# Kernel optimization log

Measured on AMD Instinct MI355X. Metric: run time of the kernel, lower is better.

The kernel has to match this reference:

```python
import jax, jax.numpy as jnp
import numpy as np

# --- constants (match init_kwargs / input_specs) ---
N_NODES = 32768   # total nodes
N_EDGES = 262144  # total edges (avg degree 8)
B = 512           # number of graphs
D = 64            # node feature / hidden dim (scalar irreps width)
DE = 16           # edge attribute dim
NEXP = 8          # num_experts
K = 2             # top-k


def setup_inputs() -> dict:
    key = jax.random.key(0)
    ks = jax.random.split(key, 20)
    x = jax.random.normal(ks[0], (N_NODES, D), dtype=jnp.float32)
    edge_src = jax.random.randint(ks[1], (N_EDGES,), 0, N_NODES, dtype=jnp.int32)
    edge_dst = jax.random.randint(ks[2], (N_EDGES,), 0, N_NODES, dtype=jnp.int32)
    edge_attr = jax.random.normal(ks[3], (N_EDGES, DE), dtype=jnp.float32)
    # sorted graph ids, every graph non-empty (64 nodes each)
    batch = jnp.repeat(jnp.arange(B, dtype=jnp.int32), N_NODES // B)
    s = 1.0 / np.sqrt(D)
    se = 1.0 / np.sqrt(DE)
    # embedding GNN params
    emb_We = jax.random.normal(ks[4], (DE, D), dtype=jnp.float32) * se
    emb_W1 = jax.random.normal(ks[5], (D, D), dtype=jnp.float32) * s
    emb_W2 = jax.random.normal(ks[6], (D, D), dtype=jnp.float32) * s
    emb_b = jnp.zeros((D,), dtype=jnp.float32)
    # gating network
    Wg = jax.random.normal(ks[7], (D, NEXP), dtype=jnp.float32) * s
    bg = jnp.zeros((NEXP,), dtype=jnp.float32)
    # stacked expert params [NEXP, ...]
    ex_We = jax.random.normal(ks[8], (NEXP, DE, D), dtype=jnp.float32) * se
    ex_W1 = jax.random.normal(ks[9], (NEXP, D, D), dtype=jnp.float32) * s
    ex_W2 = jax.random.normal(ks[10], (NEXP, D, D), dtype=jnp.float32) * s
    ex_b = jnp.zeros((NEXP, D), dtype=jnp.float32)
    ex_Wout = jax.random.normal(ks[11], (NEXP, D, 1), dtype=jnp.float32) * s
    ex_bout = jnp.zeros((NEXP, 1), dtype=jnp.float32)
    return {
        "x": x, "edge_attr": edge_attr,
        "emb_We": emb_We, "emb_W1": emb_W1, "emb_W2": emb_W2, "emb_b": emb_b,
        "Wg": Wg, "bg": bg,
        "ex_We": ex_We, "ex_W1": ex_W1, "ex_W2": ex_W2, "ex_b": ex_b,
        "ex_Wout": ex_Wout, "ex_bout": ex_bout,
        "edge_src": edge_src, "edge_dst": edge_dst, "batch": batch,
    }


def _gnn_embed(x, edge_attr, We, W1, W2, b, src, dst, batch):
    # edge-gated messages: gather x[src], modulate by projected edge attrs, scatter to dst
    msg = x[src] * (edge_attr @ We)                          # [E, D]
    agg = jax.ops.segment_sum(msg, dst, num_segments=N_NODES)  # [N, D]
    h = jax.nn.relu(x @ W1 + agg @ W2 + b)                   # [N, D]
    # mean pooling per graph
    gsum = jax.ops.segment_sum(h, batch, num_segments=B)      # [B, D]
    cnt = jax.ops.segment_sum(jnp.ones((N_NODES, 1), h.dtype), batch, num_segments=B)
    return gsum / jnp.maximum(cnt, 1.0)                      # [B, D]


def _expert(x, edge_attr, We, W1, W2, b, Wout, bout, src, dst, batch):
    emb = _gnn_embed(x, edge_attr, We, W1, W2, b, src, dst, batch)
    return emb @ Wout + bout                                  # [B, 1]


def reference(x, edge_attr, emb_We, emb_W1, emb_W2, emb_b, Wg, bg,
              ex_We, ex_W1, ex_W2, ex_b, ex_Wout, ex_bout,
              edge_src, edge_dst, batch):
    # 1) graph embeddings via embedding GNN
    graph_emb = _gnn_embed(x, edge_attr, emb_We, emb_W1, emb_W2, emb_b,
                           edge_src, edge_dst, batch)          # [B, D]
    # 2) gating: softmax over experts, top-k, renormalize
    routing_weights = jax.nn.softmax(graph_emb @ Wg + bg, axis=1)  # [B, NEXP]
    top_k_weights, top_k_indices = jax.lax.top_k(routing_weights, K)
    norm_top_k = jax.nn.softmax(top_k_weights, axis=1)             # [B, K]
    # 3) dispatch: run every expert on the full batch (vectorized equivalent of
    #    the per-expert masked sub-batch loop), then gather routed outputs
    expert_outs = jax.vmap(
        lambda We, W1, W2, b, Wo, bo: _expert(
            x, edge_attr, We, W1, W2, b, Wo, bo, edge_src, edge_dst, batch)
    )(ex_We, ex_W1, ex_W2, ex_b, ex_Wout, ex_bout)             # [NEXP, B, 1]
    per_graph = expert_outs[:, :, 0].T                         # [B, NEXP]
    gathered = jnp.take_along_axis(per_graph, top_k_indices, axis=1)  # [B, K]
    # 4) weighted combine
    final_output = jnp.sum(gathered * norm_top_k, axis=1, keepdims=True)  # [B, 1]
    return final_output, routing_weights
```

## Files before the change

### kernel.cpp

```cpp
#include <hip/hip_runtime.h>

#define N_NODES 32768
#define N_EDGES 262144
#define NB      512
#define D       64
#define DE      16
#define NEXP    8

typedef __attribute__((ext_vector_type(8))) short  short8v;
typedef __attribute__((ext_vector_type(4))) float  floatx4;

static __device__ __forceinline__ unsigned short f2bf(float f) {
  unsigned int u = __float_as_uint(f);
  u += 0x7FFFu + ((u >> 16) & 1u);
  return (unsigned short)(u >> 16);
}


__global__ void hist_kernel(const int* __restrict__ dst, int* __restrict__ counts) {
  int i = blockIdx.x * blockDim.x + threadIdx.x;
  if (i < N_EDGES) atomicAdd(&counts[dst[i]], 1);
}

__global__ void scan1_kernel(const int* __restrict__ counts, int* __restrict__ offsets,
                             int* __restrict__ bsums) {
  __shared__ int sm[256];
  int t = threadIdx.x, i = blockIdx.x * 256 + t;
  int v = counts[i];
  sm[t] = v;
  __syncthreads();
  for (int off = 1; off < 256; off <<= 1) {
    int u = (t >= off) ? sm[t - off] : 0;
    __syncthreads();
    sm[t] += u;
    __syncthreads();
  }
  offsets[i] = sm[t] - v;
  if (t == 255) bsums[blockIdx.x] = sm[255];
}

__global__ void scan2_kernel(int* __restrict__ bsums) {
  __shared__ int sm[128];
  int t = threadIdx.x;
  int v = bsums[t];
  sm[t] = v;
  __syncthreads();
  for (int off = 1; off < 128; off <<= 1) {
    int u = (t >= off) ? sm[t - off] : 0;
    __syncthreads();
    sm[t] += u;
    __syncthreads();
  }
  bsums[t] = sm[t] - v;
}

__global__ void scan3_kernel(int* __restrict__ offsets, const int* __restrict__ bsums,
                             int* __restrict__ cursor) {
  int i = blockIdx.x * 256 + threadIdx.x;
  int v = offsets[i] + bsums[blockIdx.x];
  offsets[i] = v;
  cursor[i]  = v;
  if (i == 0) offsets[N_NODES] = N_EDGES;
}

__global__ void scatter_kernel(const int* __restrict__ dst, const int* __restrict__ src,
                               const float4* __restrict__ ea4, int* __restrict__ cursor,
                               int* __restrict__ sorted_src, float4* __restrict__ sea4) {
  int i = blockIdx.x * blockDim.x + threadIdx.x;
  if (i < N_EDGES) {
    int p = atomicAdd(&cursor[dst[i]], 1);
    sorted_src[p] = src[i];
    float4 a = ea4[(size_t)i * 4 + 0];
    float4 b = ea4[(size_t)i * 4 + 1];
    float4 c = ea4[(size_t)i * 4 + 2];
    float4 d = ea4[(size_t)i * 4 + 3];
    sea4[(size_t)p * 4 + 0] = a;
    sea4[(size_t)p * 4 + 1] = b;
    sea4[(size_t)p * 4 + 2] = c;
    sea4[(size_t)p * 4 + 3] = d;
  }
}


__global__ void xconv_kernel(const float4* __restrict__ x4, ushort4* __restrict__ xb4) {
  int i = blockIdx.x * blockDim.x + threadIdx.x;
  float4 v = x4[i];
  ushort4 o;
  o.x = f2bf(v.x); o.y = f2bf(v.y); o.z = f2bf(v.z); o.w = f2bf(v.w);
  xb4[i] = o;
}

__global__ void wpack_kernel(const float* __restrict__ ex_W1, const float* __restrict__ ex_W2,
                             unsigned short* __restrict__ wpk) {
  int idx = blockIdx.x * 256 + threadIdx.x;
  int je  = idx >> 13;
  int rem = idx & 8191;
  int mat = rem >> 12;
  int cd  = rem & 4095;
  int col = cd >> 6, k = cd & 63;
  const float* W = mat ? ex_W2 : ex_W1;
  wpk[idx] = f2bf(W[je * 4096 + k * 64 + col]);
}


__global__ __launch_bounds__(256) void agg_kernel(
    const float* __restrict__ x, const int* __restrict__ sorted_src,
    const float4* __restrict__ sea4, const int* __restrict__ offsets,
    const float* __restrict__ emb_We, const float* __restrict__ ex_We,
    float* __restrict__ agg0, unsigned short* __restrict__ aggb) {
  int lane = threadIdx.x & 63;
  int n = blockIdx.x * 4 + (threadIdx.x >> 6);
  int st = offsets[n], en = offsets[n + 1];
  float t[DE];
#pragma unroll
  for (int k = 0; k < DE; ++k) t[k] = 0.f;
  for (int i = st; i < en; ++i) {
    int s = sorted_src[i];
    float xv = x[(size_t)s * D + lane];
    float4 e0 = sea4[(size_t)i * 4 + 0];
    float4 e1 = sea4[(size_t)i * 4 + 1];
    float4 e2 = sea4[(size_t)i * 4 + 2];
    float4 e3 = sea4[(size_t)i * 4 + 3];
    t[0]  += xv * e0.x; t[1]  += xv * e0.y; t[2]  += xv * e0.z; t[3]  += xv * e0.w;
    t[4]  += xv * e1.x; t[5]  += xv * e1.y; t[6]  += xv * e1.z; t[7]  += xv * e1.w;
    t[8]  += xv * e2.x; t[9]  += xv * e2.y; t[10] += xv * e2.z; t[11] += xv * e2.w;
    t[12] += xv * e3.x; t[13] += xv * e3.y; t[14] += xv * e3.z; t[15] += xv * e3.w;
  }
  {
    float a = 0.f;
#pragma unroll
    for (int k = 0; k < DE; ++k) a += t[k] * emb_We[k * D + lane];
    agg0[(size_t)n * D + lane] = a;
  }
  for (int je = 0; je < NEXP; ++je) {
    const float* We = ex_We + (size_t)je * DE * D;
    float a = 0.f;
#pragma unroll
    for (int k = 0; k < DE; ++k) a += t[k] * We[k * D + lane];
    aggb[((size_t)je * N_NODES + n) * D + lane] = f2bf(a);
  }
}


__global__ __launch_bounds__(256) void gnn0_kernel(
    const float* __restrict__ x, const float* __restrict__ agg0,
    const float* __restrict__ W1, const float* __restrict__ W2,
    const float* __restrict__ bvv, float* __restrict__ graph_emb) {
  __shared__ __align__(16) float w1s[D * D];
  __shared__ __align__(16) float w2s[D * D];
  __shared__ __align__(16) float xs[D * D];
  __shared__ __align__(16) float as2[D * D];
  int b = blockIdx.x;
  int t = threadIdx.x;
  const float4* w1src = (const float4*)W1;
  const float4* w2src = (const float4*)W2;
  const float4* xsrc  = (const float4*)(x    + (size_t)b * D * D);
  const float4* asrc  = (const float4*)(agg0 + (size_t)b * D * D);
#pragma unroll
  for (int r = 0; r < 4; ++r) {
    ((float4*)w1s)[t + r * 256] = w1src[t + r * 256];
    ((float4*)w2s)[t + r * 256] = w2src[t + r * 256];
    ((float4*)xs)[t + r * 256]  = xsrc[t + r * 256];
    ((float4*)as2)[t + r * 256] = asrc[t + r * 256];
  }
  int w = t >> 6, lane = t & 63;
  float bias = bvv[lane];
  __syncthreads();
  float pool = 0.f;
#pragma unroll
  for (int q = 0; q < 4; ++q) {
    int n0 = w * 16 + q * 4;
    float a0 = bias, a1 = bias, a2 = bias, a3 = bias;
#pragma unroll 4
    for (int c4 = 0; c4 < 16; ++c4) {
      float4 x0 = *(const float4*)&xs[(n0 + 0) * D + c4 * 4];
      float4 x1 = *(const float4*)&xs[(n0 + 1) * D + c4 * 4];
      float4 x2 = *(const float4*)&xs[(n0 + 2) * D + c4 * 4];
      float4 x3 = *(const float4*)&xs[(n0 + 3) * D + c4 * 4];
      float4 g0 = *(const float4*)&as2[(n0 + 0) * D + c4 * 4];
      float4 g1 = *(const float4*)&as2[(n0 + 1) * D + c4 * 4];
      float4 g2 = *(const float4*)&as2[(n0 + 2) * D + c4 * 4];
      float4 g3 = *(const float4*)&as2[(n0 + 3) * D + c4 * 4];
      float w10 = w1s[(c4 * 4 + 0) * D + lane];
      float w11 = w1s[(c4 * 4 + 1) * D + lane];
      float w12 = w1s[(c4 * 4 + 2) * D + lane];
      float w13 = w1s[(c4 * 4 + 3) * D + lane];
      float w20 = w2s[(c4 * 4 + 0) * D + lane];
      float w21 = w2s[(c4 * 4 + 1) * D + lane];
      float w22 = w2s[(c4 * 4 + 2) * D + lane];
      float w23 = w2s[(c4 * 4 + 3) * D + lane];
      a0 += x0.x * w10 + x0.y * w11 + x0.z * w12 + x0.w * w13
          + g0.x * w20 + g0.y * w21 + g0.z * w22 + g0.w * w23;
      a1 += x1.x * w10 + x1.y * w11 + x1.z * w12 + x1.w * w13
          + g1.x * w20 + g1.y * w21 + g1.z * w22 + g1.w * w23;
      a2 += x2.x * w10 + x2.y * w11 + x2.z * w12 + x2.w * w13
          + g2.x * w20 + g2.y * w21 + g2.z * w22 + g2.w * w23;
      a3 += x3.x * w10 + x3.y * w11 + x3.z * w12 + x3.w * w13
          + g3.x * w20 + g3.y * w21 + g3.z * w22 + g3.w * w23;
    }
    pool += fmaxf(a0, 0.f) + fmaxf(a1, 0.f) + fmaxf(a2, 0.f) + fmaxf(a3, 0.f);
  }
  __syncthreads();
  xs[w * D + lane] = pool;
  __syncthreads();
  if (w == 0) {
    float s = xs[lane] + xs[D + lane] + xs[2 * D + lane] + xs[3 * D + lane];
    graph_emb[b * D + lane] = s * (1.f / 64.f);
  }
}


__global__ __launch_bounds__(256) void gnn_mfma_kernel(
    const unsigned short* __restrict__ xb, const unsigned short* __restrict__ aggb,
    const unsigned short* __restrict__ wpk,
    const float* __restrict__ ex_b, const float* __restrict__ ex_Wout,
    const float* __restrict__ ex_bout, float* __restrict__ per_graph) {
  int g = blockIdx.x;
  int wv = threadIdx.x >> 6;
  int je = blockIdx.y * 4 + wv;
  int lane = threadIdx.x & 63;
  int r = lane & 15, q = lane >> 4;

  const short* Xb = (const short*)(xb   + (size_t)g * D * D);
  const short* Ab = (const short*)(aggb + ((size_t)je * N_NODES + (size_t)g * D) * D);
  const short* B1 = (const short*)(wpk + (size_t)je * 2 * 4096);
  const short* B2 = B1 + 4096;

  floatx4 acc[4][4];
#pragma unroll
  for (int i = 0; i < 4; ++i)
#pragma unroll
    for (int j = 0; j < 4; ++j) acc[i][j] = (floatx4){0.f, 0.f, 0.f, 0.f};

#pragma unroll
  for (int kk = 0; kk < 2; ++kk) {
    int ko = kk * 32 + q * 8;
    short8v af[4], bf[4];
#pragma unroll
    for (int rt = 0; rt < 4; ++rt) af[rt] = *(const short8v*)(Xb + (rt * 16 + r) * D + ko);
#pragma unroll
    for (int ct = 0; ct < 4; ++ct) bf[ct] = *(const short8v*)(B1 + (ct * 16 + r) * D + ko);
#pragma unroll
    for (int rt = 0; rt < 4; ++rt)
#pragma unroll
      for (int ct = 0; ct < 4; ++ct)
        acc[rt][ct] = __builtin_amdgcn_mfma_f32_16x16x32_bf16(af[rt], bf[ct], acc[rt][ct], 0, 0, 0);
  }
#pragma unroll
  for (int kk = 0; kk < 2; ++kk) {
    int ko = kk * 32 + q * 8;
    short8v af[4], bf[4];
#pragma unroll
    for (int rt = 0; rt < 4; ++rt) af[rt] = *(const short8v*)(Ab + (rt * 16 + r) * D + ko);
#pragma unroll
    for (int ct = 0; ct < 4; ++ct) bf[ct] = *(const short8v*)(B2 + (ct * 16 + r) * D + ko);
#pragma unroll
    for (int rt = 0; rt < 4; ++rt)
#pragma unroll
      for (int ct = 0; ct < 4; ++ct)
        acc[rt][ct] = __builtin_amdgcn_mfma_f32_16x16x32_bf16(af[rt], bf[ct], acc[rt][ct], 0, 0, 0);
  }

  float o = 0.f;
#pragma unroll
  for (int ct = 0; ct < 4; ++ct) {
    float bcol = ex_b[je * D + ct * 16 + r];
    float s = 0.f;
#pragma unroll
    for (int rt = 0; rt < 4; ++rt)
#pragma unroll
      for (int rg = 0; rg < 4; ++rg) s += fmaxf(acc[rt][ct][rg] + bcol, 0.f);
    s += __shfl_xor(s, 16);
    s += __shfl_xor(s, 32);
    o += s * ex_Wout[je * D + ct * 16 + r];
  }
#pragma unroll
  for (int off = 8; off >= 1; off >>= 1) o += __shfl_xor(o, off);
  if (lane == 0) per_graph[g * NEXP + je] = o * (1.f / 64.f) + ex_bout[je];
}


__global__ void gate_kernel(const float* __restrict__ graph_emb, const float* __restrict__ Wg,
                            const float* __restrict__ bg, const float* __restrict__ per_graph,
                            float* __restrict__ out) {
  __shared__ float es[D];
  __shared__ float lg[NEXP];
  int b = blockIdx.x, lane = threadIdx.x;
  es[lane] = graph_emb[b * D + lane];
  __syncthreads();
  if (lane < NEXP) {
    float v = bg[lane];
    for (int d = 0; d < D; ++d) v += es[d] * Wg[d * NEXP + lane];
    lg[lane] = v;
  }
  __syncthreads();
  float l[NEXP];
  float mx = -1e30f;
#pragma unroll
  for (int e = 0; e < NEXP; ++e) { l[e] = lg[e]; mx = fmaxf(mx, l[e]); }
  float p[NEXP];
  float sum = 0.f;
#pragma unroll
  for (int e = 0; e < NEXP; ++e) { p[e] = expf(l[e] - mx); sum += p[e]; }
  float inv = 1.f / sum;
#pragma unroll
  for (int e = 0; e < NEXP; ++e) p[e] *= inv;
  if (lane < NEXP) out[NB + b * NEXP + lane] = p[lane];
  if (lane == 0) {
    int i1 = -1; float v1 = -1e30f;
#pragma unroll
    for (int e = 0; e < NEXP; ++e) if (p[e] > v1) { v1 = p[e]; i1 = e; }
    int i2 = -1; float v2 = -1e30f;
#pragma unroll
    for (int e = 0; e < NEXP; ++e) if (e != i1 && p[e] > v2) { v2 = p[e]; i2 = e; }
    float rr = expf(v2 - v1);
    float n1 = 1.f / (1.f + rr);
    float n2 = rr / (1.f + rr);
    out[b] = n1 * per_graph[b * NEXP + i1] + n2 * per_graph[b * NEXP + i2];
  }
}


extern "C" void kernel_launch(void* const* d_in, const int* in_sizes, int n_in,
                              void* d_out, int out_size, void* d_ws, size_t ws_size,
                              hipStream_t stream) {
  const float* x         = (const float*)d_in[0];
  const float* edge_attr = (const float*)d_in[1];
  const float* emb_We    = (const float*)d_in[2];
  const float* emb_W1    = (const float*)d_in[3];
  const float* emb_W2    = (const float*)d_in[4];
  const float* emb_b     = (const float*)d_in[5];
  const float* Wg        = (const float*)d_in[6];
  const float* bg        = (const float*)d_in[7];
  const float* ex_We     = (const float*)d_in[8];
  const float* ex_W1     = (const float*)d_in[9];
  const float* ex_W2     = (const float*)d_in[10];
  const float* ex_b      = (const float*)d_in[11];
  const float* ex_Wout   = (const float*)d_in[12];
  const float* ex_bout   = (const float*)d_in[13];
  const int* edge_src    = (const int*)d_in[14];
  const int* edge_dst    = (const int*)d_in[15];

  char* p = (char*)d_ws;
  auto alloc = [&](size_t bytes) {
    char* q = p;
    p += (bytes + 255) & ~(size_t)255;
    return q;
  };
  int*   counts     = (int*)alloc((size_t)N_NODES * 4);
  int*   offsets    = (int*)alloc((size_t)(N_NODES + 1) * 4);
  int*   cursor     = (int*)alloc((size_t)N_NODES * 4);
  int*   bsums      = (int*)alloc(128 * 4);
  int*   sorted_src = (int*)alloc((size_t)N_EDGES * 4);
  float* sorted_ea  = (float*)alloc((size_t)N_EDGES * DE * 4);
  float* agg0       = (float*)alloc((size_t)N_NODES * D * 4);
  unsigned short* aggb = (unsigned short*)alloc((size_t)NEXP * N_NODES * D * 2);
  unsigned short* xb   = (unsigned short*)alloc((size_t)N_NODES * D * 2);
  unsigned short* wpk  = (unsigned short*)alloc((size_t)NEXP * 2 * D * D * 2);
  float* graph_emb  = (float*)alloc((size_t)NB * D * 4);
  float* per_graph  = (float*)alloc((size_t)NB * NEXP * 4);

  hipMemsetAsync(counts, 0, (size_t)N_NODES * 4, stream);
  hist_kernel<<<N_EDGES / 256, 256, 0, stream>>>(edge_dst, counts);
  scan1_kernel<<<N_NODES / 256, 256, 0, stream>>>(counts, offsets, bsums);
  scan2_kernel<<<1, 128, 0, stream>>>(bsums);
  scan3_kernel<<<N_NODES / 256, 256, 0, stream>>>(offsets, bsums, cursor);
  scatter_kernel<<<N_EDGES / 256, 256, 0, stream>>>(edge_dst, edge_src,
                                                    (const float4*)edge_attr, cursor,
                                                    sorted_src, (float4*)sorted_ea);
  xconv_kernel<<<(N_NODES * D / 4) / 256, 256, 0, stream>>>((const float4*)x, (ushort4*)xb);
  wpack_kernel<<<(NEXP * 2 * D * D) / 256, 256, 0, stream>>>(ex_W1, ex_W2, wpk);
  agg_kernel<<<N_NODES / 4, 256, 0, stream>>>(x, sorted_src, (const float4*)sorted_ea,
                                              offsets, emb_We, ex_We, agg0, aggb);
  gnn0_kernel<<<NB, 256, 0, stream>>>(x, agg0, emb_W1, emb_W2, emb_b, graph_emb);
  dim3 mgrid(NB, 2);
  gnn_mfma_kernel<<<mgrid, 256, 0, stream>>>(xb, aggb, wpk, ex_b, ex_Wout, ex_bout, per_graph);
  gate_kernel<<<NB, 64, 0, stream>>>(graph_emb, Wg, bg, per_graph, (float*)d_out);
}
```

Measured before the change: 257.0 us.

## Fuse x bf16 conversion into MFMA kernel via swizzled LDS; batch edge gathers

Removes the separate xconv kernel and its bf16 x buffer. The MFMA kernel now runs 512 threads per graph, one wave per expert, and first converts the graph's x tile to bf16 into XOR-swizzled shared memory that all 8 experts read. The aggregation loop is also unrolled to issue 8 neighbor index and x gathers together, exposing more memory-level parallelism. In exchange the block size grows and register pressure in the aggregation kernel rises.

```diff
diff --git a/kernel.cpp b/kernel.cpp
--- a/kernel.cpp
+++ b/kernel.cpp
@@ -81,15 +81,6 @@
   }
 }
 
-
-__global__ void xconv_kernel(const float4* __restrict__ x4, ushort4* __restrict__ xb4) {
-  int i = blockIdx.x * blockDim.x + threadIdx.x;
-  float4 v = x4[i];
-  ushort4 o;
-  o.x = f2bf(v.x); o.y = f2bf(v.y); o.z = f2bf(v.z); o.w = f2bf(v.w);
-  xb4[i] = o;
-}
-
 __global__ void wpack_kernel(const float* __restrict__ ex_W1, const float* __restrict__ ex_W2,
                              unsigned short* __restrict__ wpk) {
   int idx = blockIdx.x * 256 + threadIdx.x;
@@ -114,17 +105,28 @@
   float t[DE];
 #pragma unroll
   for (int k = 0; k < DE; ++k) t[k] = 0.f;
-  for (int i = st; i < en; ++i) {
-    int s = sorted_src[i];
-    float xv = x[(size_t)s * D + lane];
-    float4 e0 = sea4[(size_t)i * 4 + 0];
-    float4 e1 = sea4[(size_t)i * 4 + 1];
-    float4 e2 = sea4[(size_t)i * 4 + 2];
-    float4 e3 = sea4[(size_t)i * 4 + 3];
-    t[0]  += xv * e0.x; t[1]  += xv * e0.y; t[2]  += xv * e0.z; t[3]  += xv * e0.w;
-    t[4]  += xv * e1.x; t[5]  += xv * e1.y; t[6]  += xv * e1.z; t[7]  += xv * e1.w;
-    t[8]  += xv * e2.x; t[9]  += xv * e2.y; t[10] += xv * e2.z; t[11] += xv * e2.w;
-    t[12] += xv * e3.x; t[13] += xv * e3.y; t[14] += xv * e3.z; t[15] += xv * e3.w;
+
+  for (int base = st; base < en; base += 8) {
+    int m = en - base;
+    if (m > 8) m = 8;
+    int sj[8];
+#pragma unroll
+    for (int j = 0; j < 8; ++j) sj[j] = sorted_src[base + ((j < m) ? j : 0)];
+    float xv[8];
+#pragma unroll
+    for (int j = 0; j < 8; ++j) xv[j] = x[(size_t)sj[j] * D + lane];
+#pragma unroll
+    for (int j = 0; j < 8; ++j) {
+      if (j < m) {
+        const float4* ep = sea4 + ((size_t)(base + j) << 2);
+        float4 e0 = ep[0], e1 = ep[1], e2 = ep[2], e3 = ep[3];
+        float xvj = xv[j];
+        t[0]  += xvj * e0.x; t[1]  += xvj * e0.y; t[2]  += xvj * e0.z; t[3]  += xvj * e0.w;
+        t[4]  += xvj * e1.x; t[5]  += xvj * e1.y; t[6]  += xvj * e1.z; t[7]  += xvj * e1.w;
+        t[8]  += xvj * e2.x; t[9]  += xvj * e2.y; t[10] += xvj * e2.z; t[11] += xvj * e2.w;
+        t[12] += xvj * e3.x; t[13] += xvj * e3.y; t[14] += xvj * e3.z; t[15] += xvj * e3.w;
+      }
+    }
   }
   {
     float a = 0.f;
@@ -210,18 +212,32 @@
 }
 
 
-__global__ __launch_bounds__(256) void gnn_mfma_kernel(
-    const unsigned short* __restrict__ xb, const unsigned short* __restrict__ aggb,
+__global__ __launch_bounds__(512) void gnn_mfma_kernel(
+    const float* __restrict__ x, const unsigned short* __restrict__ aggb,
     const unsigned short* __restrict__ wpk,
     const float* __restrict__ ex_b, const float* __restrict__ ex_Wout,
     const float* __restrict__ ex_bout, float* __restrict__ per_graph) {
+  __shared__ __align__(16) short xls[4096];
   int g = blockIdx.x;
-  int wv = threadIdx.x >> 6;
-  int je = blockIdx.y * 4 + wv;
-  int lane = threadIdx.x & 63;
+  int t = threadIdx.x;
+  {
+    const float4* xp = (const float4*)(x + (size_t)g * 4096 + (size_t)t * 8);
+    float4 va = xp[0], vb = xp[1];
+    short8v pk;
+    pk[0] = (short)f2bf(va.x); pk[1] = (short)f2bf(va.y);
+    pk[2] = (short)f2bf(va.z); pk[3] = (short)f2bf(va.w);
+    pk[4] = (short)f2bf(vb.x); pk[5] = (short)f2bf(vb.y);
+    pk[6] = (short)f2bf(vb.z); pk[7] = (short)f2bf(vb.w);
+    int row = t >> 3, slot = t & 7;
+    *(short8v*)((char*)xls + (((row << 3) + (slot ^ (row & 7))) << 4)) = pk;
+  }
+  __syncthreads();
+
+  int wv = t >> 6;
+  int je = wv;
+  int lane = t & 63;
   int r = lane & 15, q = lane >> 4;
 
-  const short* Xb = (const short*)(xb   + (size_t)g * D * D);
   const short* Ab = (const short*)(aggb + ((size_t)je * N_NODES + (size_t)g * D) * D);
   const short* B1 = (const short*)(wpk + (size_t)je * 2 * 4096);
   const short* B2 = B1 + 4096;
@@ -237,7 +253,11 @@
     int ko = kk * 32 + q * 8;
     short8v af[4], bf[4];
 #pragma unroll
-    for (int rt = 0; rt < 4; ++rt) af[rt] = *(const short8v*)(Xb + (rt * 16 + r) * D + ko);
+    for (int rt = 0; rt < 4; ++rt) {
+      int row = rt * 16 + r;
+      int slot = kk * 4 + q;
+      af[rt] = *(const short8v*)((char*)xls + (((row << 3) + (slot ^ (row & 7))) << 4));
+    }
 #pragma unroll
     for (int ct = 0; ct < 4; ++ct) bf[ct] = *(const short8v*)(B1 + (ct * 16 + r) * D + ko);
 #pragma unroll
@@ -355,7 +375,6 @@
   float* sorted_ea  = (float*)alloc((size_t)N_EDGES * DE * 4);
   float* agg0       = (float*)alloc((size_t)N_NODES * D * 4);
   unsigned short* aggb = (unsigned short*)alloc((size_t)NEXP * N_NODES * D * 2);
-  unsigned short* xb   = (unsigned short*)alloc((size_t)N_NODES * D * 2);
   unsigned short* wpk  = (unsigned short*)alloc((size_t)NEXP * 2 * D * D * 2);
   float* graph_emb  = (float*)alloc((size_t)NB * D * 4);
   float* per_graph  = (float*)alloc((size_t)NB * NEXP * 4);
@@ -368,12 +387,10 @@
   scatter_kernel<<<N_EDGES / 256, 256, 0, stream>>>(edge_dst, edge_src,
                                                     (const float4*)edge_attr, cursor,
                                                     sorted_src, (float4*)sorted_ea);
-  xconv_kernel<<<(N_NODES * D / 4) / 256, 256, 0, stream>>>((const float4*)x, (ushort4*)xb);
   wpack_kernel<<<(NEXP * 2 * D * D) / 256, 256, 0, stream>>>(ex_W1, ex_W2, wpk);
   agg_kernel<<<N_NODES / 4, 256, 0, stream>>>(x, sorted_src, (const float4*)sorted_ea,
                                               offsets, emb_We, ex_We, agg0, aggb);
   gnn0_kernel<<<NB, 256, 0, stream>>>(x, agg0, emb_W1, emb_W2, emb_b, graph_emb);
-  dim3 mgrid(NB, 2);
-  gnn_mfma_kernel<<<mgrid, 256, 0, stream>>>(xb, aggb, wpk, ex_b, ex_Wout, ex_bout, per_graph);
+  gnn_mfma_kernel<<<NB, 512, 0, stream>>>(x, aggb, wpk, ex_b, ex_Wout, ex_bout, per_graph);
   gate_kernel<<<NB, 64, 0, stream>>>(graph_emb, Wg, bg, per_graph, (float*)d_out);
 }
```

After: 246.3 us. 1.04x faster.
